# Kernel tuning notes

Hardware: AMD Instinct MI355X
Metric: run time of the kernel (lower is better)

The kernel has to match this reference:

```python
import jax, jax.numpy as jnp
import numpy as np

C_CODE, F_OUT, K_TOP, M_GRP, GROUPS, STRIDE, KSZ = 64, 256, 4, 8, 8, 4, 4
B, W, H = 4, 64, 64


def setup_inputs() -> dict:
    key = jax.random.key(0)
    k1, k2, k3, k4, k5 = jax.random.split(key, 5)
    shape = (B, K_TOP, M_GRP, W, H)
    ind_pos = jax.random.randint(k1, shape, 0, C_CODE, dtype=jnp.int32)
    ind_neg = jax.random.randint(k2, shape, 0, C_CODE, dtype=jnp.int32)
    val_pos = jax.random.normal(k3, shape, dtype=jnp.float32)
    val_neg = jax.random.normal(k4, shape, dtype=jnp.float32)
    # torch conv_transpose2d weight layout: [Cin, Cout/groups, kh, kw]
    weight = jax.random.normal(k5, (C_CODE * M_GRP, F_OUT // GROUPS, KSZ, KSZ), dtype=jnp.float32) * 0.05
    return {"ind_pos": ind_pos, "ind_neg": ind_neg, "val_pos": val_pos, "val_neg": val_neg, "weight": weight}


def _deindex_and_deconv(ind_pos, ind_neg, val_pos, val_neg, weight):
    b, k, m, w, h = ind_pos.shape
    c = C_CODE
    # offset each m-group's indices into the flattened c*m channel axis
    offs = (c * jnp.arange(m, dtype=jnp.int32)).reshape(1, 1, m, 1, 1)
    ip = (ind_pos + offs).reshape(b, k * m, w, h)
    iN = (ind_neg + offs).reshape(b, k * m, w, h)
    vp = val_pos.reshape(b, k * m, w, h)
    vn = val_neg.reshape(b, k * m, w, h)
    bb = jnp.arange(b).reshape(b, 1, 1, 1)
    ww = jnp.arange(w).reshape(1, 1, w, 1)
    hh = jnp.arange(h).reshape(1, 1, 1, h)
    out = jnp.zeros((b, c * m, w, h), dtype=vp.dtype)
    out = out.at[bb, ip, ww, hh].set(vp)  # scatter pos values along channel dim
    out = out.at[bb, iN, ww, hh].set(vn)  # neg scatter second (overwrites ties, like torch)
    # conv_transpose2d(stride=STRIDE, padding=0, groups=GROUPS) as dilated conv:
    # rearrange torch weight [Cin, Cout/g, kh, kw] -> OIHW [Cout, Cin/g, kh, kw], flip spatial
    cin, cog, kh, kw = weight.shape
    g = GROUPS
    rhs = weight.reshape(g, cin // g, cog, kh, kw).transpose(0, 2, 1, 3, 4).reshape(g * cog, cin // g, kh, kw)
    rhs = rhs[:, :, ::-1, ::-1]
    y = jax.lax.conv_general_dilated(
        out, rhs,
        window_strides=(1, 1),
        padding=[(kh - 1, kh - 1), (kw - 1, kw - 1)],
        lhs_dilation=(STRIDE, STRIDE),
        dimension_numbers=("NCHW", "OIHW", "NCHW"),
        feature_group_count=g,
    )
    return y


def reference(ind_pos, ind_neg, val_pos, val_neg, weight):
    return _deindex_and_deconv(ind_pos, ind_neg, val_pos, val_neg, weight)
```

## Files before the change

### kernel.cpp

```cpp
#include <hip/hip_runtime.h>


typedef float f32x4  __attribute__((ext_vector_type(4)));
typedef short bf16x8 __attribute__((ext_vector_type(8)));

__device__ __forceinline__ unsigned short f32_to_bf16_rne(float f) {
    unsigned int u = __float_as_uint(f);
    return (unsigned short)((u + 0x7FFFu + ((u >> 16) & 1u)) >> 16);
}

__global__ __launch_bounds__(256) void wt_transpose_kernel(
    const float* __restrict__ weight, unsigned short* __restrict__ ws)
{
    __shared__ unsigned short stile[64 * 72];
    const int m    = blockIdx.x >> 3;
    const int pblk = blockIdx.x & 7;
    const int t    = threadIdx.x;
    const int p    = t & 63;
    const int chi  = t >> 6;
    #pragma unroll
    for (int r = 0; r < 16; ++r) {
        const int c = chi * 16 + r;
        const float v = weight[(size_t)(64 * m + c) * 512 + pblk * 64 + p];
        stile[p * 72 + c] = f32_to_bf16_rne(v);
    }
    __syncthreads();
    uint4* dst4 = (uint4*)(ws + (size_t)(m * 512 + pblk * 64) * 64);
    #pragma unroll
    for (int pass = 0; pass < 2; ++pass) {
        const int g = pass * 256 + t;
        const uint4 v = *(const uint4*)(stile + (g >> 3) * 72 + (g & 7) * 8);
        dst4[g] = v;
    }
}

__global__ __launch_bounds__(256) void convdeidx_mfma_kernel(
    const int* __restrict__ ind_pos, const int* __restrict__ ind_neg,
    const float* __restrict__ val_pos, const float* __restrict__ val_neg,
    const unsigned short* __restrict__ ws, float* __restrict__ out)
{
    __shared__ unsigned short sA[256 * 72];
    __shared__ unsigned short sX[64 * 72];
    __shared__ int2 spair[64 * 10];


    const int bi  = blockIdx.x;
    const int w   = bi & 63;
    const int m   = (bi >> 6) & 7;
    const int b   = bi >> 9;
    const int tid = threadIdx.x;
    const int wid = tid >> 6, lane = tid & 63;
    const int q   = lane >> 4, ln = lane & 15;

    {
        const int k = tid >> 6, h = tid & 63;
        const int idx = (((b * 4 + k) * 8 + m) * 64 + w) * 64 + h;
        spair[h * 10 + k]     = make_int2(ind_pos[idx], __float_as_int(val_pos[idx]));
        spair[h * 10 + 4 + k] = make_int2(ind_neg[idx], __float_as_int(val_neg[idx]));
    }
    {
        uint4* x4 = (uint4*)sX;
        const uint4 z = make_uint4(0u, 0u, 0u, 0u);
        x4[tid] = z;
        x4[tid + 256] = z;
        if (tid < 64) x4[tid + 512] = z;
    }
    const uint4* wsrc4 = (const uint4*)(ws + (size_t)m * 512 * 64);
    #pragma unroll
    for (int r = 0; r < 8; ++r) {
        const int g = r * 256 + tid;
        const uint4 v = wsrc4[g];
        *(uint4*)(sA + (g >> 3) * 72 + (g & 7) * 8) = v;
    }
    __syncthreads();

    if (tid < 64) {
        const int h = tid;
        #pragma unroll
        for (int p = 0; p < 8; ++p) {
            const int2 pr = spair[h * 10 + p];
            sX[h * 72 + pr.x] = f32_to_bf16_rne(__int_as_float(pr.y));
        }
    }
    __syncthreads();

    f32x4* outv = (f32x4*)out;

    #pragma unroll
    for (int chunk = 0; chunk < 2; ++chunk) {
        if (chunk == 1) {
            __syncthreads();
            #pragma unroll
            for (int r = 0; r < 8; ++r) {
                const int g = r * 256 + tid;
                const uint4 v = wsrc4[2048 + g];
                *(uint4*)(sA + (g >> 3) * 72 + (g & 7) * 8) = v;
            }
            __syncthreads();
        }

        f32x4 acc[4][4];
        #pragma unroll
        for (int mt = 0; mt < 4; ++mt)
            #pragma unroll
            for (int nt = 0; nt < 4; ++nt)
                acc[mt][nt] = (f32x4){0.f, 0.f, 0.f, 0.f};

        #pragma unroll
        for (int kt = 0; kt < 2; ++kt) {
            bf16x8 afr[4], bfr[4];
            #pragma unroll
            for (int mt = 0; mt < 4; ++mt)
                afr[mt] = *(const bf16x8*)(sA + (wid * 64 + mt * 16 + ln) * 72 + (kt * 4 + q) * 8);
            #pragma unroll
            for (int nt = 0; nt < 4; ++nt)
                bfr[nt] = *(const bf16x8*)(sX + (nt * 16 + ln) * 72 + (kt * 4 + q) * 8);
            #pragma unroll
            for (int mt = 0; mt < 4; ++mt)
                #pragma unroll
                for (int nt = 0; nt < 4; ++nt)
                    acc[mt][nt] = __builtin_amdgcn_mfma_f32_16x16x32_bf16(
                        afr[mt], bfr[nt], acc[mt][nt], 0, 0, 0);
        }

        const int ocg0 = chunk * 16 + wid * 4;
        #pragma unroll
        for (int mt = 0; mt < 4; ++mt) {
            const size_t rowbase =
                ((size_t)(b * 256 + m * 32 + ocg0 + mt) * 256 + (w * 4 + q)) * 64;
            #pragma unroll
            for (int nt = 0; nt < 4; ++nt)
                __builtin_nontemporal_store(acc[mt][nt], outv + rowbase + nt * 16 + ln);
        }
    }
}

extern "C" void kernel_launch(void* const* d_in, const int* in_sizes, int n_in,
                              void* d_out, int out_size, void* d_ws, size_t ws_size,
                              hipStream_t stream) {
    const int*   ind_pos = (const int*)  d_in[0];
    const int*   ind_neg = (const int*)  d_in[1];
    const float* val_pos = (const float*)d_in[2];
    const float* val_neg = (const float*)d_in[3];
    const float* weight  = (const float*)d_in[4];
    float*       y       = (float*)d_out;
    unsigned short* ws   = (unsigned short*)d_ws;

    hipLaunchKernelGGL(wt_transpose_kernel, dim3(64), dim3(256), 0, stream, weight, ws);
    hipLaunchKernelGGL(convdeidx_mfma_kernel, dim3(2048), dim3(256), 0, stream,
                       ind_pos, ind_neg, val_pos, val_neg, ws, y);
}
```

Before: 283.5 us.

## Process four w rows per block to reuse staged weight tiles

Each block now handles four consecutive w positions instead of one, so the grid shrinks by a factor of four. The bf16 weight tile is loaded into shared memory once and its A fragments are kept in registers across all four w rows. This amortises the weight traffic and the per-block setup. The sparse scatter now has all 256 threads writing directly from registers, which removes the spair staging buffer. The trade-off is fewer blocks (512) for occupancy on the GPU, a larger sX buffer, and more registers held live.

```diff
diff --git a/kernel.cpp b/kernel.cpp
--- a/kernel.cpp
+++ b/kernel.cpp
@@ -40,31 +40,35 @@
     const unsigned short* __restrict__ ws, float* __restrict__ out)
 {
     __shared__ unsigned short sA[256 * 72];
-    __shared__ unsigned short sX[64 * 72];
-    __shared__ int2 spair[64 * 10];
-
+    __shared__ unsigned short sX[4 * 64 * 72];
 
     const int bi  = blockIdx.x;
-    const int w   = bi & 63;
-    const int m   = (bi >> 6) & 7;
-    const int b   = bi >> 9;
+    const int wg  = bi & 15;
+    const int m   = (bi >> 4) & 7;
+    const int b   = bi >> 7;
+    const int w0  = wg * 4;
     const int tid = threadIdx.x;
     const int wid = tid >> 6, lane = tid & 63;
     const int q   = lane >> 4, ln = lane & 15;
 
-    {
-        const int k = tid >> 6, h = tid & 63;
-        const int idx = (((b * 4 + k) * 8 + m) * 64 + w) * 64 + h;
-        spair[h * 10 + k]     = make_int2(ind_pos[idx], __float_as_int(val_pos[idx]));
-        spair[h * 10 + 4 + k] = make_int2(ind_neg[idx], __float_as_int(val_neg[idx]));
+    const int wl = tid >> 6;
+    const int h  = tid & 63;
+    int   ipos[4], ineg[4];
+    float vpos[4], vneg[4];
+    #pragma unroll
+    for (int k = 0; k < 4; ++k) {
+        const size_t idx = ((((size_t)b * 4 + k) * 8 + m) * 64 + (w0 + wl)) * 64 + h;
+        ipos[k] = ind_pos[idx]; vpos[k] = val_pos[idx];
+        ineg[k] = ind_neg[idx]; vneg[k] = val_neg[idx];
     }
+
     {
         uint4* x4 = (uint4*)sX;
         const uint4 z = make_uint4(0u, 0u, 0u, 0u);
-        x4[tid] = z;
-        x4[tid + 256] = z;
-        if (tid < 64) x4[tid + 512] = z;
+        #pragma unroll
+        for (int r = 0; r < 9; ++r) x4[r * 256 + tid] = z;
     }
+
     const uint4* wsrc4 = (const uint4*)(ws + (size_t)m * 512 * 64);
     #pragma unroll
     for (int r = 0; r < 8; ++r) {
@@ -74,13 +78,12 @@
     }
     __syncthreads();
 
-    if (tid < 64) {
-        const int h = tid;
+    {
+        unsigned short* xrow = sX + (wl * 64 + h) * 72;
         #pragma unroll
-        for (int p = 0; p < 8; ++p) {
-            const int2 pr = spair[h * 10 + p];
-            sX[h * 72 + pr.x] = f32_to_bf16_rne(__int_as_float(pr.y));
-        }
+        for (int k = 0; k < 4; ++k) xrow[ipos[k]] = f32_to_bf16_rne(vpos[k]);
+        #pragma unroll
+        for (int k = 0; k < 4; ++k) xrow[ineg[k]] = f32_to_bf16_rne(vneg[k]);
     }
     __syncthreads();
 
@@ -99,38 +102,48 @@
             __syncthreads();
         }
 
-        f32x4 acc[4][4];
+        bf16x8 afr[2][4];
         #pragma unroll
-        for (int mt = 0; mt < 4; ++mt)
+        for (int kt = 0; kt < 2; ++kt)
             #pragma unroll
-            for (int nt = 0; nt < 4; ++nt)
-                acc[mt][nt] = (f32x4){0.f, 0.f, 0.f, 0.f};
+            for (int mt = 0; mt < 4; ++mt)
+                afr[kt][mt] = *(const bf16x8*)(sA + (wid * 64 + mt * 16 + ln) * 72 + (kt * 4 + q) * 8);
+
+        const int ocg0 = chunk * 16 + wid * 4;
 
         #pragma unroll
-        for (int kt = 0; kt < 2; ++kt) {
-            bf16x8 afr[4], bfr[4];
+        for (int ww = 0; ww < 4; ++ww) {
+            bf16x8 bfr[2][4];
             #pragma unroll
-            for (int mt = 0; mt < 4; ++mt)
-                afr[mt] = *(const bf16x8*)(sA + (wid * 64 + mt * 16 + ln) * 72 + (kt * 4 + q) * 8);
-            #pragma unroll
-            for (int nt = 0; nt < 4; ++nt)
-                bfr[nt] = *(const bf16x8*)(sX + (nt * 16 + ln) * 72 + (kt * 4 + q) * 8);
+            for (int kt = 0; kt < 2; ++kt)
+                #pragma unroll
+                for (int nt = 0; nt < 4; ++nt)
+                    bfr[kt][nt] = *(const bf16x8*)(sX + (ww * 64 + nt * 16 + ln) * 72 + (kt * 4 + q) * 8);
+
+            f32x4 acc[4][4];
             #pragma unroll
             for (int mt = 0; mt < 4; ++mt)
                 #pragma unroll
                 for (int nt = 0; nt < 4; ++nt)
-                    acc[mt][nt] = __builtin_amdgcn_mfma_f32_16x16x32_bf16(
-                        afr[mt], bfr[nt], acc[mt][nt], 0, 0, 0);
-        }
+                    acc[mt][nt] = (f32x4){0.f, 0.f, 0.f, 0.f};
 
-        const int ocg0 = chunk * 16 + wid * 4;
-        #pragma unroll
-        for (int mt = 0; mt < 4; ++mt) {
-            const size_t rowbase =
-                ((size_t)(b * 256 + m * 32 + ocg0 + mt) * 256 + (w * 4 + q)) * 64;
             #pragma unroll
-            for (int nt = 0; nt < 4; ++nt)
-                __builtin_nontemporal_store(acc[mt][nt], outv + rowbase + nt * 16 + ln);
+            for (int kt = 0; kt < 2; ++kt)
+                #pragma unroll
+                for (int mt = 0; mt < 4; ++mt)
+                    #pragma unroll
+                    for (int nt = 0; nt < 4; ++nt)
+                        acc[mt][nt] = __builtin_amdgcn_mfma_f32_16x16x32_bf16(
+                            afr[kt][mt], bfr[kt][nt], acc[mt][nt], 0, 0, 0);
+
+            #pragma unroll
+            for (int mt = 0; mt < 4; ++mt) {
+                const size_t rowbase =
+                    ((size_t)(b * 256 + m * 32 + ocg0 + mt) * 256 + ((w0 + ww) * 4 + q)) * 64;
+                #pragma unroll
+                for (int nt = 0; nt < 4; ++nt)
+                    __builtin_nontemporal_store(acc[mt][nt], outv + rowbase + nt * 16 + ln);
+            }
         }
     }
 }
@@ -147,6 +160,6 @@
     unsigned short* ws   = (unsigned short*)d_ws;
 
     hipLaunchKernelGGL(wt_transpose_kernel, dim3(64), dim3(256), 0, stream, weight, ws);
-    hipLaunchKernelGGL(convdeidx_mfma_kernel, dim3(2048), dim3(256), 0, stream,
+    hipLaunchKernelGGL(convdeidx_mfma_kernel, dim3(512), dim3(256), 0, stream,
                        ind_pos, ind_neg, val_pos, val_neg, ws, y);
 }
```

Result: no change. 288.4 us (+1.7%).
